# Optimization experiments

Measured on AMD Instinct MI355X. Metric: run time of the kernel, lower is better.

The kernel has to match this reference:

```python
import jax, jax.numpy as jnp
import numpy as np

B, C, I, E = 2048, 128, 16, 10            # nodes, channels, irreps_in dim (lmax=3 -> 1+3+5+7), elements
M0, K3_0, K2_0, K1_0 = 1, 23, 4, 1        # output 0e: irrep dim, num_paths per correlation order 3/2/1
M1, K3_1, K2_1, K1_1 = 3, 33, 5, 1        # output 1o


def setup_inputs() -> dict:
    key = jax.random.key(0)
    ks = jax.random.split(key, 16)
    g = lambda k, s, sc=1.0: jax.random.normal(k, s, jnp.float32) * sc
    x = g(ks[0], (B, C, I))
    # node_attrs: one-hot chemical element per node
    y = jax.nn.one_hot(jax.random.randint(ks[1], (B,), 0, E), E, dtype=jnp.float32)
    return dict(
        x=x, y=y,
        U3_0=g(ks[2], (M0, I, I, I, K3_0), 0.1), U2_0=g(ks[3], (M0, I, I, K2_0), 0.1),
        U1_0=g(ks[4], (M0, I, K1_0), 0.1),
        W3_0=g(ks[5], (E, K3_0, C), 0.05), W2_0=g(ks[6], (E, K2_0, C), 0.05),
        W1_0=g(ks[7], (E, K1_0, C), 0.05),
        U3_1=g(ks[8], (M1, I, I, I, K3_1), 0.1), U2_1=g(ks[9], (M1, I, I, K2_1), 0.1),
        U1_1=g(ks[10], (M1, I, K1_1), 0.1),
        W3_1=g(ks[11], (E, K3_1, C), 0.05), W2_1=g(ks[12], (E, K2_1, C), 0.05),
        W1_1=g(ks[13], (E, K1_1, C), 0.05),
    )


def _contraction(x, y, U3, U2, U1, W3, W2, W1):
    # MACE Contraction for one output irrep.
    # x: [b,c,i] node features, y: [b,e] one-hot element attrs.
    # main: einsum('...ik,ekc,bci,be->bc...') for correlation order 3
    wy3 = jnp.einsum("ekc,be->bkc", W3, y)                 # per-node selected weights [b,k,c]
    t = jnp.einsum("bkc,bci->bkci", wy3, x)                # [b,k,c,i]
    out = jnp.einsum("mijlk,bkci->bcmjl", U3, t)           # main contraction -> [b,c,m,j,l]
    # order 2: weighting ('...k,ekc,be->bc...') then feature contraction ('bc...i,bci->bc...')
    wy2 = jnp.einsum("ekc,be->bkc", W2, y)
    out = out + jnp.einsum("mjlk,bkc->bcmjl", U2, wy2)
    out = jnp.einsum("bcmji,bci->bcmj", out, x)            # [b,c,m,j]
    # order 1
    wy1 = jnp.einsum("ekc,be->bkc", W1, y)
    out = out + jnp.einsum("mjk,bkc->bcmj", U1, wy1)
    out = jnp.einsum("bcmi,bci->bcm", out, x)              # [b,c,m]
    return out.reshape(out.shape[0], -1)                    # [b, c*m]


def reference(x, y, U3_0, U2_0, U1_0, W3_0, W2_0, W1_0,
              U3_1, U2_1, U1_1, W3_1, W2_1, W1_1):
    out0 = _contraction(x, y, U3_0, U2_0, U1_0, W3_0, W2_0, W1_0)   # 0e -> [b, c]
    out1 = _contraction(x, y, U3_1, U2_1, U1_1, W3_1, W2_1, W1_1)   # 1o -> [b, 3c]
    return jnp.concatenate([out0, out1], axis=-1)                    # [b, 4c]
```

## Files before the change

kernel.cpp:

```cpp
#include <hip/hip_runtime.h>
#include <hip/hip_fp16.h>
#include <stdint.h>


#define BN 2048
#define CN 128
#define EN 10

#define NT3 816
#define NT2 136
#define NTT (NT3 + NT2 + 16)
#define K3_0 23
#define K3_1 33
#define K2_0 4
#define K2_1 5

#define U3S0_OFF 0
#define U3S1_OFF (K3_0*NT3)
#define U2S0_OFF (U3S1_OFF + 3*K3_1*NT3)
#define U2S1_OFF (U2S0_OFF + K2_0*NT2)
#define LISTS_OFF (U2S1_OFF + 3*K2_1*NT2)
#define CNT_OFF (LISTS_OFF + EN*BN)
#define TALL_OFF (((CNT_OFF + EN) + 3) & ~3)
#define WS_NEED_BYTES ((size_t)TALL_OFF*4 + (size_t)EN*CN*NTT*8)

#define PREP_TOT (K3_0*NT3 + 3*K3_1*NT3 + K2_0*NT2 + 3*K2_1*NT2)
#define PREP_BLOCKS ((PREP_TOT + 255) / 256)

typedef float v2f __attribute__((ext_vector_type(2)));
#define FMA2(a, b, c) __builtin_elementwise_fma((a), (b), (c))
static __device__ __forceinline__ v2f splat2(float v) { v2f r; r.x = v; r.y = v; return r; }

__global__ __launch_bounds__(256) void prep_sym(
    const float* __restrict__ U3_0, const float* __restrict__ U2_0,
    const float* __restrict__ U3_1, const float* __restrict__ U2_1,
    const float* __restrict__ yg, float* __restrict__ ws)
{
    const int bid = blockIdx.x, tid = threadIdx.x;
    if (bid < PREP_BLOCKS) {
        const int N0 = K3_0*NT3, N1 = 3*K3_1*NT3, P0 = K2_0*NT2;
        const int it = bid*256 + tid;
        if (it >= PREP_TOT) return;
        if (it < N0 + N1) {
            const float* U3; int m, k, K, t, dst;
            if (it < N0) { U3 = U3_0; K = K3_0; m = 0; k = it / NT3; t = it - k*NT3; dst = U3S0_OFF + it; }
            else { int r = it - N0; U3 = U3_1; K = K3_1; int mk = r / NT3; t = r - mk*NT3;
                   m = mk / K3_1; k = mk - m*K3_1; dst = U3S1_OFF + r; }
            int a = 0, rem = t;
            while (rem >= ((16-a)*(17-a))/2) { rem -= ((16-a)*(17-a))/2; ++a; }
            int b = a;
            while (rem >= 16-b) { rem -= 16-b; ++b; }
            const int cc = b + rem;
            #define AT3(i,j,l) U3[(size_t)(((m*16+(i))*16+(j))*16+(l))*K + k]
            float D = AT3(a,b,cc) + AT3(a,cc,b) + AT3(b,a,cc)
                    + AT3(b,cc,a) + AT3(cc,a,b) + AT3(cc,b,a);
            #undef AT3
            const int eq = (a==b) + (b==cc);
            D *= (eq==2) ? (1.f/6.f) : (eq==1) ? 0.5f : 1.f;
            ws[dst] = D;
        } else {
            const int it2 = it - (N0+N1);
            const float* U2; int m, k, K, pr, dst;
            if (it2 < P0) { U2 = U2_0; K = K2_0; m = 0; k = it2 / NT2; pr = it2 - k*NT2; dst = U2S0_OFF + it2; }
            else { int r = it2 - P0; U2 = U2_1; K = K2_1; int mk = r / NT2; pr = r - mk*NT2;
                   m = mk / K2_1; k = mk - m*K2_1; dst = U2S1_OFF + r; }
            int a = 0, rem = pr;
            while (rem >= 16-a) { rem -= 16-a; ++a; }
            const int b = a + rem;
            float D = U2[(size_t)((m*16+a)*16+b)*K + k]
                    + U2[(size_t)((m*16+b)*16+a)*K + k];
            if (a == b) D *= 0.5f;
            ws[dst] = D;
        }
    } else if (bid < PREP_BLOCKS + EN) {
        const int e = bid - PREP_BLOCKS;
        __shared__ int lcnt;
        if (tid == 0) lcnt = 0;
        __syncthreads();
        int* lists = (int*)(ws + LISTS_OFF);
        for (int b = tid; b < BN; b += 256) {
            if (yg[b*EN + e] > 0.5f) {
                int p = atomicAdd(&lcnt, 1);
                lists[e*BN + p] = b;
            }
        }
        __syncthreads();
        if (tid == 0) ((int*)(ws + CNT_OFF))[e] = lcnt;
    }
}

static __device__ __forceinline__ uint2 pack_h4(float a0, float a1, float a2, float a3) {
    __half2 lo = __floats2half2_rn(a0, a1);
    __half2 hi = __floats2half2_rn(a2, a3);
    uint2 r;
    r.x = *reinterpret_cast<const unsigned int*>(&lo);
    r.y = *reinterpret_cast<const unsigned int*>(&hi);
    return r;
}

__global__ __launch_bounds__(128) void sc_build(
    const float* __restrict__ usym, uint2* __restrict__ tall,
    const float* __restrict__ U1_0, const float* __restrict__ U1_1,
    const float* __restrict__ W3_0, const float* __restrict__ W2_0, const float* __restrict__ W1_0,
    const float* __restrict__ W3_1, const float* __restrict__ W2_1, const float* __restrict__ W1_1)
{
    const int g0 = blockIdx.x * 8;
    const int e = blockIdx.y;
    const int c = threadIdx.x;
    uint2* out8 = tall + (size_t)(e*CN + c)*NTT;

    if (g0 < NT3) {
        float w0[K3_0], w1[K3_1];
#pragma unroll
        for (int k = 0; k < K3_0; ++k) w0[k] = W3_0[(e*K3_0 + k)*CN + c];
#pragma unroll
        for (int k = 0; k < K3_1; ++k) w1[k] = W3_1[(e*K3_1 + k)*CN + c];
        const float* u0 = usym + U3S0_OFF;
        const float* u1 = usym + U3S1_OFF;
#pragma unroll 2
        for (int j = 0; j < 8; ++j) {
            const int g = g0 + j;
            float a0 = 0.f, a1 = 0.f, a2 = 0.f, a3 = 0.f;
#pragma unroll
            for (int k = 0; k < K3_0; ++k) a0 = fmaf(u0[k*NT3 + g], w0[k], a0);
#pragma unroll
            for (int k = 0; k < K3_1; ++k) {
                a1 = fmaf(u1[k*NT3 + g], w1[k], a1);
                a2 = fmaf(u1[(K3_1 + k)*NT3 + g], w1[k], a2);
                a3 = fmaf(u1[(2*K3_1 + k)*NT3 + g], w1[k], a3);
            }
            out8[g] = pack_h4(a0, a1, a2, a3);
        }
    } else if (g0 < NT3 + NT2) {
        float w0[K2_0], w1[K2_1];
#pragma unroll
        for (int k = 0; k < K2_0; ++k) w0[k] = W2_0[(e*K2_0 + k)*CN + c];
#pragma unroll
        for (int k = 0; k < K2_1; ++k) w1[k] = W2_1[(e*K2_1 + k)*CN + c];
        const float* u0 = usym + U2S0_OFF;
        const float* u1 = usym + U2S1_OFF;
#pragma unroll
        for (int j = 0; j < 8; ++j) {
            const int g = g0 + j;
            const int pr = g - NT3;
            float a0 = 0.f, a1 = 0.f, a2 = 0.f, a3 = 0.f;
#pragma unroll
            for (int k = 0; k < K2_0; ++k) a0 = fmaf(u0[k*NT2 + pr], w0[k], a0);
#pragma unroll
            for (int k = 0; k < K2_1; ++k) {
                a1 = fmaf(u1[k*NT2 + pr], w1[k], a1);
                a2 = fmaf(u1[(K2_1 + k)*NT2 + pr], w1[k], a2);
                a3 = fmaf(u1[(2*K2_1 + k)*NT2 + pr], w1[k], a3);
            }
            out8[g] = pack_h4(a0, a1, a2, a3);
        }
    } else {
        const float w10 = W1_0[e*CN + c];
        const float w11 = W1_1[e*CN + c];
#pragma unroll
        for (int j = 0; j < 8; ++j) {
            const int g = g0 + j;
            const int a = g - (NT3 + NT2);
            out8[g] = pack_h4(U1_0[a]*w10, U1_1[a]*w11,
                              U1_1[16+a]*w11, U1_1[32+a]*w11);
        }
    }
}

__global__ __launch_bounds__(128) void sc_apply(
    const float* __restrict__ xg, const float* __restrict__ ws,
    float* __restrict__ outg)
{
    const int c = blockIdx.x, e = blockIdx.y, tid = threadIdx.x;
    __shared__ uint2 Tsh[NTT];
    __shared__ v2f xs[16*128];

    const uint2* __restrict__ tG =
        (const uint2*)(ws + TALL_OFF) + (size_t)(e*CN + c)*NTT;
    for (int i = tid; i < NTT; i += 128) Tsh[i] = tG[i];

    const int* lists = (const int*)(ws + LISTS_OFF) + e*BN;
    const int cnt = ((const int*)(ws + CNT_OFF))[e];
    __syncthreads();

    for (int base = 0; base < cnt; base += 256) {
        const int s0 = base + tid, s1 = base + tid + 128;
        const bool act0 = s0 < cnt, act1 = s1 < cnt;
        const int n0 = lists[act0 ? s0 : 0];
        const int n1 = lists[act1 ? s1 : 0];
        const float4* p0 = (const float4*)(xg + ((size_t)n0*CN + c)*16);
        const float4* p1 = (const float4*)(xg + ((size_t)n1*CN + c)*16);
#pragma unroll
        for (int d = 0; d < 4; ++d) {
            const float4 v0 = p0[d]; const float4 v1 = p1[d];
            v2f w;
            w.x = v0.x; w.y = v1.x; xs[(4*d+0)*128+tid] = w;
            w.x = v0.y; w.y = v1.y; xs[(4*d+1)*128+tid] = w;
            w.x = v0.z; w.y = v1.z; xs[(4*d+2)*128+tid] = w;
            w.x = v0.w; w.y = v1.w; xs[(4*d+3)*128+tid] = w;
        }

        v2f acc0 = splat2(0.f), acc1 = acc0, acc2 = acc0, acc3 = acc0;
        int t3 = 0, t2 = NT3;
#pragma unroll 1
        for (int a = 0; a < 16; ++a) {
            const v2f xa = xs[a*128+tid];
            const uint2 t1w = Tsh[NT3 + NT2 + a];
            const float2 t1lo = __half22float2(*reinterpret_cast<const __half2*>(&t1w.x));
            const float2 t1hi = __half22float2(*reinterpret_cast<const __half2*>(&t1w.y));
            v2f tP0 = splat2(t1lo.x), tP1 = splat2(t1lo.y),
                tP2 = splat2(t1hi.x), tP3 = splat2(t1hi.y);
#pragma unroll 1
            for (int b = a; b < 16; ++b) {
                const v2f xb = xs[b*128+tid];
                const uint2 c2w = Tsh[t2]; ++t2;
                const float2 c2lo = __half22float2(*reinterpret_cast<const __half2*>(&c2w.x));
                const float2 c2hi = __half22float2(*reinterpret_cast<const __half2*>(&c2w.y));
                v2f tB0 = splat2(c2lo.x), tB1 = splat2(c2lo.y),
                    tB2 = splat2(c2hi.x), tB3 = splat2(c2hi.y);
#pragma unroll 4
                for (int cc = b; cc < 16; ++cc) {
                    const v2f xc = xs[cc*128+tid];
                    const uint2 c3w = Tsh[t3]; ++t3;
                    const float2 c3lo = __half22float2(*reinterpret_cast<const __half2*>(&c3w.x));
                    const float2 c3hi = __half22float2(*reinterpret_cast<const __half2*>(&c3w.y));
                    tB0 = FMA2(splat2(c3lo.x), xc, tB0);
                    tB1 = FMA2(splat2(c3lo.y), xc, tB1);
                    tB2 = FMA2(splat2(c3hi.x), xc, tB2);
                    tB3 = FMA2(splat2(c3hi.y), xc, tB3);
                }
                tP0 = FMA2(tB0, xb, tP0);
                tP1 = FMA2(tB1, xb, tP1);
                tP2 = FMA2(tB2, xb, tP2);
                tP3 = FMA2(tB3, xb, tP3);
            }
            acc0 = FMA2(tP0, xa, acc0);
            acc1 = FMA2(tP1, xa, acc1);
            acc2 = FMA2(tP2, xa, acc2);
            acc3 = FMA2(tP3, xa, acc3);
        }
        if (act0) {
            float* o = outg + (size_t)n0*512;
            o[c] = acc0.x;
            o[128 + c*3 + 0] = acc1.x; o[128 + c*3 + 1] = acc2.x; o[128 + c*3 + 2] = acc3.x;
        }
        if (act1) {
            float* o = outg + (size_t)n1*512;
            o[c] = acc0.y;
            o[128 + c*3 + 0] = acc1.y; o[128 + c*3 + 1] = acc2.y; o[128 + c*3 + 2] = acc3.y;
        }
    }
}

__global__ __launch_bounds__(128) void sc_main_fused(
    const float* __restrict__ xg,
    const float* __restrict__ U1_0, const float* __restrict__ U1_1,
    const float* __restrict__ W3_0, const float* __restrict__ W2_0, const float* __restrict__ W1_0,
    const float* __restrict__ W3_1, const float* __restrict__ W2_1, const float* __restrict__ W1_1,
    const float* __restrict__ ws, float* __restrict__ outg)
{
    const int c = blockIdx.x, e = blockIdx.y, tid = threadIdx.x;
    __shared__ float4 T3s[NT3];
    __shared__ float4 T2s[NT2];
    __shared__ float4 T1s[16];
    __shared__ float xs0[16*128];
    __shared__ float xs1[16*128];
    __shared__ float wk30s[K3_0], wk31s[K3_1], wk20s[K2_0], wk21s[K2_1];

    if (tid < K3_0) wk30s[tid] = W3_0[(e*K3_0 + tid)*CN + c];
    if (tid >= 32 && tid < 32 + K3_1) wk31s[tid-32] = W3_1[(e*K3_1 + (tid-32))*CN + c];
    if (tid >= 72 && tid < 72 + K2_0) wk20s[tid-72] = W2_0[(e*K2_0 + (tid-72))*CN + c];
    if (tid >= 80 && tid < 80 + K2_1) wk21s[tid-80] = W2_1[(e*K2_1 + (tid-80))*CN + c];
    __syncthreads();

    const float* u3s0 = ws + U3S0_OFF;
    const float* u3s1 = ws + U3S1_OFF;
    for (int g = tid; g < NT3/4; g += 128) {
        float4 A0 = make_float4(0,0,0,0), A1 = A0, A2 = A0, A3 = A0;
#pragma unroll
        for (int k = 0; k < K3_0; ++k) {
            const float w = wk30s[k];
            const float4 u = ((const float4*)(u3s0 + k*NT3))[g];
            A0.x = fmaf(u.x, w, A0.x); A0.y = fmaf(u.y, w, A0.y);
            A0.z = fmaf(u.z, w, A0.z); A0.w = fmaf(u.w, w, A0.w);
        }
#pragma unroll 8
        for (int k = 0; k < K3_1; ++k) {
            const float w = wk31s[k];
            const float4 ua = ((const float4*)(u3s1 + k*NT3))[g];
            A1.x = fmaf(ua.x, w, A1.x); A1.y = fmaf(ua.y, w, A1.y);
            A1.z = fmaf(ua.z, w, A1.z); A1.w = fmaf(ua.w, w, A1.w);
            const float4 ub = ((const float4*)(u3s1 + (K3_1 + k)*NT3))[g];
            A2.x = fmaf(ub.x, w, A2.x); A2.y = fmaf(ub.y, w, A2.y);
            A2.z = fmaf(ub.z, w, A2.z); A2.w = fmaf(ub.w, w, A2.w);
            const float4 uc = ((const float4*)(u3s1 + (2*K3_1 + k)*NT3))[g];
            A3.x = fmaf(uc.x, w, A3.x); A3.y = fmaf(uc.y, w, A3.y);
            A3.z = fmaf(uc.z, w, A3.z); A3.w = fmaf(uc.w, w, A3.w);
        }
        T3s[4*g+0] = make_float4(A0.x, A1.x, A2.x, A3.x);
        T3s[4*g+1] = make_float4(A0.y, A1.y, A2.y, A3.y);
        T3s[4*g+2] = make_float4(A0.z, A1.z, A2.z, A3.z);
        T3s[4*g+3] = make_float4(A0.w, A1.w, A2.w, A3.w);
    }
    const float* u2s0 = ws + U2S0_OFF;
    const float* u2s1 = ws + U2S1_OFF;
    for (int g = tid; g < NT2/4; g += 128) {
        float4 A0 = make_float4(0,0,0,0), A1 = A0, A2 = A0, A3 = A0;
#pragma unroll
        for (int k = 0; k < K2_0; ++k) {
            const float w = wk20s[k];
            const float4 u = ((const float4*)(u2s0 + k*NT2))[g];
            A0.x = fmaf(u.x, w, A0.x); A0.y = fmaf(u.y, w, A0.y);
            A0.z = fmaf(u.z, w, A0.z); A0.w = fmaf(u.w, w, A0.w);
        }
#pragma unroll
        for (int k = 0; k < K2_1; ++k) {
            const float w = wk21s[k];
            const float4 ua = ((const float4*)(u2s1 + k*NT2))[g];
            A1.x = fmaf(ua.x, w, A1.x); A1.y = fmaf(ua.y, w, A1.y);
            A1.z = fmaf(ua.z, w, A1.z); A1.w = fmaf(ua.w, w, A1.w);
            const float4 ub = ((const float4*)(u2s1 + (K2_1 + k)*NT2))[g];
            A2.x = fmaf(ub.x, w, A2.x); A2.y = fmaf(ub.y, w, A2.y);
            A2.z = fmaf(ub.z, w, A2.z); A2.w = fmaf(ub.w, w, A2.w);
            const float4 uc = ((const float4*)(u2s1 + (2*K2_1 + k)*NT2))[g];
            A3.x = fmaf(uc.x, w, A3.x); A3.y = fmaf(uc.y, w, A3.y);
            A3.z = fmaf(uc.z, w, A3.z); A3.w = fmaf(uc.w, w, A3.w);
        }
        T2s[4*g+0] = make_float4(A0.x, A1.x, A2.x, A3.x);
        T2s[4*g+1] = make_float4(A0.y, A1.y, A2.y, A3.y);
        T2s[4*g+2] = make_float4(A0.z, A1.z, A2.z, A3.z);
        T2s[4*g+3] = make_float4(A0.w, A1.w, A2.w, A3.w);
    }
    if (tid < 16) {
        const float wk10 = W1_0[e*CN + c];
        const float wk11 = W1_1[e*CN + c];
        const int j = tid;
        T1s[j] = make_float4(U1_0[j]*wk10, U1_1[j]*wk11,
                             U1_1[16+j]*wk11, U1_1[32+j]*wk11);
    }

    const int* lists = (const int*)(ws + LISTS_OFF) + e*BN;
    const int cnt = ((const int*)(ws + CNT_OFF))[e];
    __syncthreads();

    for (int base = 0; base < cnt; base += 256) {
        const int s0 = base + tid, s1 = base + tid + 128;
        const bool act0 = s0 < cnt, act1 = s1 < cnt;
        const int n0 = lists[act0 ? s0 : 0];
        const int n1 = lists[act1 ? s1 : 0];
        const float4* p0 = (const float4*)(xg + ((size_t)n0*CN + c)*16);
        const float4* p1 = (const float4*)(xg + ((size_t)n1*CN + c)*16);
#pragma unroll
        for (int d = 0; d < 4; ++d) {
            const float4 v0 = p0[d]; const float4 v1 = p1[d];
            xs0[(4*d+0)*128+tid] = v0.x; xs0[(4*d+1)*128+tid] = v0.y;
            xs0[(4*d+2)*128+tid] = v0.z; xs0[(4*d+3)*128+tid] = v0.w;
            xs1[(4*d+0)*128+tid] = v1.x; xs1[(4*d+1)*128+tid] = v1.y;
            xs1[(4*d+2)*128+tid] = v1.z; xs1[(4*d+3)*128+tid] = v1.w;
        }
        float4 acc0 = make_float4(0,0,0,0), acc1 = acc0;
        int t3 = 0, t2i = 0;
#pragma unroll 1
        for (int a = 0; a < 16; ++a) {
            const float xa0 = xs0[a*128+tid];
            const float xa1 = xs1[a*128+tid];
            float4 tP0 = T1s[a], tP1 = tP0;
#pragma unroll 1
            for (int b = a; b < 16; ++b) {
                const float xb0 = xs0[b*128+tid];
                const float xb1 = xs1[b*128+tid];
                const float4 c2v = T2s[t2i]; ++t2i;
                float4 tB0 = c2v, tB1 = c2v;
#pragma unroll 4
                for (int cc = b; cc < 16; ++cc) {
                    const float xc0 = xs0[cc*128+tid];
                    const float xc1 = xs1[cc*128+tid];
                    const float4 c3v = T3s[t3]; ++t3;
                    tB0.x = fmaf(c3v.x, xc0, tB0.x); tB0.y = fmaf(c3v.y, xc0, tB0.y);
                    tB0.z = fmaf(c3v.z, xc0, tB0.z); tB0.w = fmaf(c3v.w, xc0, tB0.w);
                    tB1.x = fmaf(c3v.x, xc1, tB1.x); tB1.y = fmaf(c3v.y, xc1, tB1.y);
                    tB1.z = fmaf(c3v.z, xc1, tB1.z); tB1.w = fmaf(c3v.w, xc1, tB1.w);
                }
                tP0.x = fmaf(tB0.x, xb0, tP0.x); tP0.y = fmaf(tB0.y, xb0, tP0.y);
                tP0.z = fmaf(tB0.z, xb0, tP0.z); tP0.w = fmaf(tB0.w, xb0, tP0.w);
                tP1.x = fmaf(tB1.x, xb1, tP1.x); tP1.y = fmaf(tB1.y, xb1, tP1.y);
                tP1.z = fmaf(tB1.z, xb1, tP1.z); tP1.w = fmaf(tB1.w, xb1, tP1.w);
            }
            acc0.x = fmaf(tP0.x, xa0, acc0.x); acc0.y = fmaf(tP0.y, xa0, acc0.y);
            acc0.z = fmaf(tP0.z, xa0, acc0.z); acc0.w = fmaf(tP0.w, xa0, acc0.w);
            acc1.x = fmaf(tP1.x, xa1, acc1.x); acc1.y = fmaf(tP1.y, xa1, acc1.y);
            acc1.z = fmaf(tP1.z, xa1, acc1.z); acc1.w = fmaf(tP1.w, xa1, acc1.w);
        }
        if (act0) {
            float* o = outg + (size_t)n0*512;
            o[c] = acc0.x;
            o[128 + c*3 + 0] = acc0.y; o[128 + c*3 + 1] = acc0.z; o[128 + c*3 + 2] = acc0.w;
        }
        if (act1) {
            float* o = outg + (size_t)n1*512;
            o[c] = acc1.x;
            o[128 + c*3 + 0] = acc1.y; o[128 + c*3 + 1] = acc1.z; o[128 + c*3 + 2] = acc1.w;
        }
    }
}

extern "C" void kernel_launch(void* const* d_in, const int* in_sizes, int n_in,
                              void* d_out, int out_size, void* d_ws, size_t ws_size,
                              hipStream_t stream) {
    const float* x = (const float*)d_in[0];
    const float* y = (const float*)d_in[1];
    const float* U3_0 = (const float*)d_in[2];
    const float* U2_0 = (const float*)d_in[3];
    const float* U1_0 = (const float*)d_in[4];
    const float* W3_0 = (const float*)d_in[5];
    const float* W2_0 = (const float*)d_in[6];
    const float* W1_0 = (const float*)d_in[7];
    const float* U3_1 = (const float*)d_in[8];
    const float* U2_1 = (const float*)d_in[9];
    const float* U1_1 = (const float*)d_in[10];
    const float* W3_1 = (const float*)d_in[11];
    const float* W2_1 = (const float*)d_in[12];
    const float* W1_1 = (const float*)d_in[13];
    float* out = (float*)d_out;
    float* ws = (float*)d_ws;

    prep_sym<<<dim3(PREP_BLOCKS + EN), 256, 0, stream>>>(U3_0, U2_0, U3_1, U2_1, y, ws);
    if (ws_size >= WS_NEED_BYTES) {
        sc_build<<<dim3(NTT/8, EN), 128, 0, stream>>>(ws, (uint2*)(ws + TALL_OFF),
                                                      U1_0, U1_1,
                                                      W3_0, W2_0, W1_0, W3_1, W2_1, W1_1);
        sc_apply<<<dim3(CN, EN), 128, 0, stream>>>(x, ws, out);
    } else {
        sc_main_fused<<<dim3(CN, EN), 128, 0, stream>>>(x, U1_0, U1_1,
                                                        W3_0, W2_0, W1_0,
                                                        W3_1, W2_1, W1_1, ws, out);
    }
}
```

Before: 209.3 us.

## Fuse symmetrization prep into build kernel and use scalar FMAs in apply

Removes the separate prep_sym launch on the main path. The build kernel now reads the raw U3/U2 tensors directly, sums the six (or two) index permutations with the per-element weights, and also builds the per-element node lists in an extra block column. The apply kernel replaces packed v2f FMAs with scalar fmaf on separate accumulators. This saves one kernel launch and the intermediate usym round trip, but the build does six times more strided U3 reads per output.

```diff
diff --git a/kernel.cpp b/kernel.cpp
--- a/kernel.cpp
+++ b/kernel.cpp
@@ -15,21 +15,236 @@
 #define K2_0 4
 #define K2_1 5
 
+#define TALL2F 20490
+#define WS2_NEED_BYTES ((size_t)TALL2F*4 + (size_t)EN*CN*NTT*8)
+
 #define U3S0_OFF 0
 #define U3S1_OFF (K3_0*NT3)
 #define U2S0_OFF (U3S1_OFF + 3*K3_1*NT3)
 #define U2S1_OFF (U2S0_OFF + K2_0*NT2)
 #define LISTS_OFF (U2S1_OFF + 3*K2_1*NT2)
 #define CNT_OFF (LISTS_OFF + EN*BN)
-#define TALL_OFF (((CNT_OFF + EN) + 3) & ~3)
-#define WS_NEED_BYTES ((size_t)TALL_OFF*4 + (size_t)EN*CN*NTT*8)
-
+#define WSF_NEED_BYTES ((size_t)(CNT_OFF + EN) * 4)
 #define PREP_TOT (K3_0*NT3 + 3*K3_1*NT3 + K2_0*NT2 + 3*K2_1*NT2)
 #define PREP_BLOCKS ((PREP_TOT + 255) / 256)
 
 typedef float v2f __attribute__((ext_vector_type(2)));
-#define FMA2(a, b, c) __builtin_elementwise_fma((a), (b), (c))
-static __device__ __forceinline__ v2f splat2(float v) { v2f r; r.x = v; r.y = v; return r; }
+
+static __device__ __forceinline__ uint2 pack_h4(float a0, float a1, float a2, float a3) {
+    __half2 lo = __floats2half2_rn(a0, a1);
+    __half2 hi = __floats2half2_rn(a2, a3);
+    uint2 r;
+    r.x = *reinterpret_cast<const unsigned int*>(&lo);
+    r.y = *reinterpret_cast<const unsigned int*>(&hi);
+    return r;
+}
+
+static __device__ __forceinline__ void acc_perm3(
+    const float* __restrict__ U3_0, const float* __restrict__ U3_1, int idx,
+    const float (&w0)[K3_0], const float (&w1)[K3_1],
+    float& s0, float& s1, float& s2, float& s3)
+{
+    const float* u0p = U3_0 + idx * K3_0;
+#pragma unroll
+    for (int k = 0; k < K3_0; ++k) s0 = fmaf(u0p[k], w0[k], s0);
+    const float* u1p = U3_1 + (size_t)idx * K3_1;
+#pragma unroll
+    for (int k = 0; k < K3_1; ++k) {
+        const float wv = w1[k];
+        s1 = fmaf(u1p[k], wv, s1);
+        s2 = fmaf(u1p[135168 + k], wv, s2);
+        s3 = fmaf(u1p[270336 + k], wv, s3);
+    }
+}
+
+__global__ __launch_bounds__(128) void build_fused(
+    const float* __restrict__ U3_0, const float* __restrict__ U2_0, const float* __restrict__ U1_0,
+    const float* __restrict__ U3_1, const float* __restrict__ U2_1, const float* __restrict__ U1_1,
+    const float* __restrict__ W3_0, const float* __restrict__ W2_0, const float* __restrict__ W1_0,
+    const float* __restrict__ W3_1, const float* __restrict__ W2_1, const float* __restrict__ W1_1,
+    const float* __restrict__ yg, float* __restrict__ ws)
+{
+    const int gx = blockIdx.x, e = blockIdx.y, tid = threadIdx.x;
+    if (gx == 121) {
+        __shared__ int lcnt;
+        if (tid == 0) lcnt = 0;
+        __syncthreads();
+        int* lists = (int*)ws;
+        for (int b = tid; b < BN; b += 128) {
+            if (yg[b * EN + e] > 0.5f) {
+                int p = atomicAdd(&lcnt, 1);
+                lists[e * BN + p] = b;
+            }
+        }
+        __syncthreads();
+        if (tid == 0) ((int*)ws)[EN * BN + e] = lcnt;
+        return;
+    }
+
+    const int g0 = gx * 8;
+    const int c = tid;
+    uint2* out8 = (uint2*)(ws + TALL2F) + (size_t)(e * CN + c) * NTT;
+
+    if (g0 < NT3) {
+        float w0[K3_0], w1[K3_1];
+#pragma unroll
+        for (int k = 0; k < K3_0; ++k) w0[k] = W3_0[(e * K3_0 + k) * CN + c];
+#pragma unroll
+        for (int k = 0; k < K3_1; ++k) w1[k] = W3_1[(e * K3_1 + k) * CN + c];
+#pragma unroll 1
+        for (int j = 0; j < 8; ++j) {
+            const int g = g0 + j;
+            int a = 0, rem = g;
+            while (rem >= ((16 - a) * (17 - a)) / 2) { rem -= ((16 - a) * (17 - a)) / 2; ++a; }
+            int b = a;
+            while (rem >= 16 - b) { rem -= 16 - b; ++b; }
+            const int cc = b + rem;
+            float s0 = 0.f, s1 = 0.f, s2 = 0.f, s3 = 0.f;
+            acc_perm3(U3_0, U3_1, (a * 16 + b) * 16 + cc, w0, w1, s0, s1, s2, s3);
+            acc_perm3(U3_0, U3_1, (a * 16 + cc) * 16 + b, w0, w1, s0, s1, s2, s3);
+            acc_perm3(U3_0, U3_1, (b * 16 + a) * 16 + cc, w0, w1, s0, s1, s2, s3);
+            acc_perm3(U3_0, U3_1, (b * 16 + cc) * 16 + a, w0, w1, s0, s1, s2, s3);
+            acc_perm3(U3_0, U3_1, (cc * 16 + a) * 16 + b, w0, w1, s0, s1, s2, s3);
+            acc_perm3(U3_0, U3_1, (cc * 16 + b) * 16 + a, w0, w1, s0, s1, s2, s3);
+            const int eq = (a == b) + (b == cc);
+            const float sc = (eq == 2) ? (1.f / 6.f) : (eq == 1) ? 0.5f : 1.f;
+            out8[g] = pack_h4(s0 * sc, s1 * sc, s2 * sc, s3 * sc);
+        }
+    } else if (g0 < NT3 + NT2) {
+        float w0[K2_0], w1[K2_1];
+#pragma unroll
+        for (int k = 0; k < K2_0; ++k) w0[k] = W2_0[(e * K2_0 + k) * CN + c];
+#pragma unroll
+        for (int k = 0; k < K2_1; ++k) w1[k] = W2_1[(e * K2_1 + k) * CN + c];
+#pragma unroll 1
+        for (int j = 0; j < 8; ++j) {
+            const int g = g0 + j;
+            int a = 0, rem = g - NT3;
+            while (rem >= 16 - a) { rem -= 16 - a; ++a; }
+            const int b = a + rem;
+            float s0 = 0.f, s1 = 0.f, s2 = 0.f, s3 = 0.f;
+#pragma unroll
+            for (int p = 0; p < 2; ++p) {
+                const int i = p ? b : a, jj = p ? a : b;
+                const float* u0p = U2_0 + (i * 16 + jj) * K2_0;
+#pragma unroll
+                for (int k = 0; k < K2_0; ++k) s0 = fmaf(u0p[k], w0[k], s0);
+                const float* u1p = U2_1 + (i * 16 + jj) * K2_1;
+#pragma unroll
+                for (int k = 0; k < K2_1; ++k) {
+                    const float wv = w1[k];
+                    s1 = fmaf(u1p[k], wv, s1);
+                    s2 = fmaf(u1p[1280 + k], wv, s2);
+                    s3 = fmaf(u1p[2560 + k], wv, s3);
+                }
+            }
+            const float sc = (a == b) ? 0.5f : 1.f;
+            out8[g] = pack_h4(s0 * sc, s1 * sc, s2 * sc, s3 * sc);
+        }
+    } else {
+        const float w10 = W1_0[e * CN + c];
+        const float w11 = W1_1[e * CN + c];
+#pragma unroll
+        for (int j = 0; j < 8; ++j) {
+            const int g = g0 + j;
+            const int a = g - (NT3 + NT2);
+            out8[g] = pack_h4(U1_0[a] * w10, U1_1[a] * w11,
+                              U1_1[16 + a] * w11, U1_1[32 + a] * w11);
+        }
+    }
+}
+
+__global__ __launch_bounds__(128) void sc_apply(
+    const float* __restrict__ xg, const float* __restrict__ ws,
+    float* __restrict__ outg)
+{
+    const int c = blockIdx.x, e = blockIdx.y, tid = threadIdx.x;
+    __shared__ uint2 Tsh[NTT];
+    __shared__ v2f xs[16 * 128];
+
+    const uint2* __restrict__ tG =
+        (const uint2*)(ws + TALL2F) + (size_t)(e * CN + c) * NTT;
+    for (int i = tid; i < NTT; i += 128) Tsh[i] = tG[i];
+
+    const int* lists = (const int*)ws + e * BN;
+    const int cnt = ((const int*)ws)[EN * BN + e];
+    __syncthreads();
+
+    for (int base = 0; base < cnt; base += 256) {
+        const int s0 = base + tid, s1 = base + tid + 128;
+        const bool act0 = s0 < cnt, act1 = s1 < cnt;
+        const int n0 = lists[act0 ? s0 : 0];
+        const int n1 = lists[act1 ? s1 : 0];
+        const float4* p0 = (const float4*)(xg + ((size_t)n0 * CN + c) * 16);
+        const float4* p1 = (const float4*)(xg + ((size_t)n1 * CN + c) * 16);
+#pragma unroll
+        for (int d = 0; d < 4; ++d) {
+            const float4 v0 = p0[d]; const float4 v1 = p1[d];
+            v2f w;
+            w.x = v0.x; w.y = v1.x; xs[(4 * d + 0) * 128 + tid] = w;
+            w.x = v0.y; w.y = v1.y; xs[(4 * d + 1) * 128 + tid] = w;
+            w.x = v0.z; w.y = v1.z; xs[(4 * d + 2) * 128 + tid] = w;
+            w.x = v0.w; w.y = v1.w; xs[(4 * d + 3) * 128 + tid] = w;
+        }
+
+        float acc00 = 0.f, acc01 = 0.f, acc10 = 0.f, acc11 = 0.f;
+        float acc20 = 0.f, acc21 = 0.f, acc30 = 0.f, acc31 = 0.f;
+        int t3 = 0, t2 = NT3;
+#pragma unroll 1
+        for (int a = 0; a < 16; ++a) {
+            const v2f xa = xs[a * 128 + tid];
+            const uint2 t1w = Tsh[NT3 + NT2 + a];
+            const __half2 t1A = *reinterpret_cast<const __half2*>(&t1w.x);
+            const __half2 t1B = *reinterpret_cast<const __half2*>(&t1w.y);
+            float tP00 = __low2float(t1A), tP10 = __high2float(t1A);
+            float tP20 = __low2float(t1B), tP30 = __high2float(t1B);
+            float tP01 = tP00, tP11 = tP10, tP21 = tP20, tP31 = tP30;
+#pragma unroll 1
+            for (int b = a; b < 16; ++b) {
+                const v2f xb = xs[b * 128 + tid];
+                const uint2 c2w = Tsh[t2]; ++t2;
+                const __half2 c2A = *reinterpret_cast<const __half2*>(&c2w.x);
+                const __half2 c2B = *reinterpret_cast<const __half2*>(&c2w.y);
+                float tB00 = __low2float(c2A), tB10 = __high2float(c2A);
+                float tB20 = __low2float(c2B), tB30 = __high2float(c2B);
+                float tB01 = tB00, tB11 = tB10, tB21 = tB20, tB31 = tB30;
+#pragma unroll 4
+                for (int cc = b; cc < 16; ++cc) {
+                    const v2f xc = xs[cc * 128 + tid];
+                    const uint2 w = Tsh[t3]; ++t3;
+                    const __half2 hA = *reinterpret_cast<const __half2*>(&w.x);
+                    const __half2 hB = *reinterpret_cast<const __half2*>(&w.y);
+                    tB00 = fmaf(__low2float(hA),  xc.x, tB00);
+                    tB01 = fmaf(__low2float(hA),  xc.y, tB01);
+                    tB10 = fmaf(__high2float(hA), xc.x, tB10);
+                    tB11 = fmaf(__high2float(hA), xc.y, tB11);
+                    tB20 = fmaf(__low2float(hB),  xc.x, tB20);
+                    tB21 = fmaf(__low2float(hB),  xc.y, tB21);
+                    tB30 = fmaf(__high2float(hB), xc.x, tB30);
+                    tB31 = fmaf(__high2float(hB), xc.y, tB31);
+                }
+                tP00 = fmaf(tB00, xb.x, tP00); tP01 = fmaf(tB01, xb.y, tP01);
+                tP10 = fmaf(tB10, xb.x, tP10); tP11 = fmaf(tB11, xb.y, tP11);
+                tP20 = fmaf(tB20, xb.x, tP20); tP21 = fmaf(tB21, xb.y, tP21);
+                tP30 = fmaf(tB30, xb.x, tP30); tP31 = fmaf(tB31, xb.y, tP31);
+            }
+            acc00 = fmaf(tP00, xa.x, acc00); acc01 = fmaf(tP01, xa.y, acc01);
+            acc10 = fmaf(tP10, xa.x, acc10); acc11 = fmaf(tP11, xa.y, acc11);
+            acc20 = fmaf(tP20, xa.x, acc20); acc21 = fmaf(tP21, xa.y, acc21);
+            acc30 = fmaf(tP30, xa.x, acc30); acc31 = fmaf(tP31, xa.y, acc31);
+        }
+        if (act0) {
+            float* o = outg + (size_t)n0 * 512;
+            o[c] = acc00;
+            o[128 + c * 3 + 0] = acc10; o[128 + c * 3 + 1] = acc20; o[128 + c * 3 + 2] = acc30;
+        }
+        if (act1) {
+            float* o = outg + (size_t)n1 * 512;
+            o[c] = acc01;
+            o[128 + c * 3 + 0] = acc11; o[128 + c * 3 + 1] = acc21; o[128 + c * 3 + 2] = acc31;
+        }
+    }
+}
 
 __global__ __launch_bounds__(256) void prep_sym(
     const float* __restrict__ U3_0, const float* __restrict__ U2_0,
@@ -89,169 +304,6 @@
     }
 }
 
-static __device__ __forceinline__ uint2 pack_h4(float a0, float a1, float a2, float a3) {
-    __half2 lo = __floats2half2_rn(a0, a1);
-    __half2 hi = __floats2half2_rn(a2, a3);
-    uint2 r;
-    r.x = *reinterpret_cast<const unsigned int*>(&lo);
-    r.y = *reinterpret_cast<const unsigned int*>(&hi);
-    return r;
-}
-
-__global__ __launch_bounds__(128) void sc_build(
-    const float* __restrict__ usym, uint2* __restrict__ tall,
-    const float* __restrict__ U1_0, const float* __restrict__ U1_1,
-    const float* __restrict__ W3_0, const float* __restrict__ W2_0, const float* __restrict__ W1_0,
-    const float* __restrict__ W3_1, const float* __restrict__ W2_1, const float* __restrict__ W1_1)
-{
-    const int g0 = blockIdx.x * 8;
-    const int e = blockIdx.y;
-    const int c = threadIdx.x;
-    uint2* out8 = tall + (size_t)(e*CN + c)*NTT;
-
-    if (g0 < NT3) {
-        float w0[K3_0], w1[K3_1];
-#pragma unroll
-        for (int k = 0; k < K3_0; ++k) w0[k] = W3_0[(e*K3_0 + k)*CN + c];
-#pragma unroll
-        for (int k = 0; k < K3_1; ++k) w1[k] = W3_1[(e*K3_1 + k)*CN + c];
-        const float* u0 = usym + U3S0_OFF;
-        const float* u1 = usym + U3S1_OFF;
-#pragma unroll 2
-        for (int j = 0; j < 8; ++j) {
-            const int g = g0 + j;
-            float a0 = 0.f, a1 = 0.f, a2 = 0.f, a3 = 0.f;
-#pragma unroll
-            for (int k = 0; k < K3_0; ++k) a0 = fmaf(u0[k*NT3 + g], w0[k], a0);
-#pragma unroll
-            for (int k = 0; k < K3_1; ++k) {
-                a1 = fmaf(u1[k*NT3 + g], w1[k], a1);
-                a2 = fmaf(u1[(K3_1 + k)*NT3 + g], w1[k], a2);
-                a3 = fmaf(u1[(2*K3_1 + k)*NT3 + g], w1[k], a3);
-            }
-            out8[g] = pack_h4(a0, a1, a2, a3);
-        }
-    } else if (g0 < NT3 + NT2) {
-        float w0[K2_0], w1[K2_1];
-#pragma unroll
-        for (int k = 0; k < K2_0; ++k) w0[k] = W2_0[(e*K2_0 + k)*CN + c];
-#pragma unroll
-        for (int k = 0; k < K2_1; ++k) w1[k] = W2_1[(e*K2_1 + k)*CN + c];
-        const float* u0 = usym + U2S0_OFF;
-        const float* u1 = usym + U2S1_OFF;
-#pragma unroll
-        for (int j = 0; j < 8; ++j) {
-            const int g = g0 + j;
-            const int pr = g - NT3;
-            float a0 = 0.f, a1 = 0.f, a2 = 0.f, a3 = 0.f;
-#pragma unroll
-            for (int k = 0; k < K2_0; ++k) a0 = fmaf(u0[k*NT2 + pr], w0[k], a0);
-#pragma unroll
-            for (int k = 0; k < K2_1; ++k) {
-                a1 = fmaf(u1[k*NT2 + pr], w1[k], a1);
-                a2 = fmaf(u1[(K2_1 + k)*NT2 + pr], w1[k], a2);
-                a3 = fmaf(u1[(2*K2_1 + k)*NT2 + pr], w1[k], a3);
-            }
-            out8[g] = pack_h4(a0, a1, a2, a3);
-        }
-    } else {
-        const float w10 = W1_0[e*CN + c];
-        const float w11 = W1_1[e*CN + c];
-#pragma unroll
-        for (int j = 0; j < 8; ++j) {
-            const int g = g0 + j;
-            const int a = g - (NT3 + NT2);
-            out8[g] = pack_h4(U1_0[a]*w10, U1_1[a]*w11,
-                              U1_1[16+a]*w11, U1_1[32+a]*w11);
-        }
-    }
-}
-
-__global__ __launch_bounds__(128) void sc_apply(
-    const float* __restrict__ xg, const float* __restrict__ ws,
-    float* __restrict__ outg)
-{
-    const int c = blockIdx.x, e = blockIdx.y, tid = threadIdx.x;
-    __shared__ uint2 Tsh[NTT];
-    __shared__ v2f xs[16*128];
-
-    const uint2* __restrict__ tG =
-        (const uint2*)(ws + TALL_OFF) + (size_t)(e*CN + c)*NTT;
-    for (int i = tid; i < NTT; i += 128) Tsh[i] = tG[i];
-
-    const int* lists = (const int*)(ws + LISTS_OFF) + e*BN;
-    const int cnt = ((const int*)(ws + CNT_OFF))[e];
-    __syncthreads();
-
-    for (int base = 0; base < cnt; base += 256) {
-        const int s0 = base + tid, s1 = base + tid + 128;
-        const bool act0 = s0 < cnt, act1 = s1 < cnt;
-        const int n0 = lists[act0 ? s0 : 0];
-        const int n1 = lists[act1 ? s1 : 0];
-        const float4* p0 = (const float4*)(xg + ((size_t)n0*CN + c)*16);
-        const float4* p1 = (const float4*)(xg + ((size_t)n1*CN + c)*16);
-#pragma unroll
-        for (int d = 0; d < 4; ++d) {
-            const float4 v0 = p0[d]; const float4 v1 = p1[d];
-            v2f w;
-            w.x = v0.x; w.y = v1.x; xs[(4*d+0)*128+tid] = w;
-            w.x = v0.y; w.y = v1.y; xs[(4*d+1)*128+tid] = w;
-            w.x = v0.z; w.y = v1.z; xs[(4*d+2)*128+tid] = w;
-            w.x = v0.w; w.y = v1.w; xs[(4*d+3)*128+tid] = w;
-        }
-
-        v2f acc0 = splat2(0.f), acc1 = acc0, acc2 = acc0, acc3 = acc0;
-        int t3 = 0, t2 = NT3;
-#pragma unroll 1
-        for (int a = 0; a < 16; ++a) {
-            const v2f xa = xs[a*128+tid];
-            const uint2 t1w = Tsh[NT3 + NT2 + a];
-            const float2 t1lo = __half22float2(*reinterpret_cast<const __half2*>(&t1w.x));
-            const float2 t1hi = __half22float2(*reinterpret_cast<const __half2*>(&t1w.y));
-            v2f tP0 = splat2(t1lo.x), tP1 = splat2(t1lo.y),
-                tP2 = splat2(t1hi.x), tP3 = splat2(t1hi.y);
-#pragma unroll 1
-            for (int b = a; b < 16; ++b) {
-                const v2f xb = xs[b*128+tid];
-                const uint2 c2w = Tsh[t2]; ++t2;
-                const float2 c2lo = __half22float2(*reinterpret_cast<const __half2*>(&c2w.x));
-                const float2 c2hi = __half22float2(*reinterpret_cast<const __half2*>(&c2w.y));
-                v2f tB0 = splat2(c2lo.x), tB1 = splat2(c2lo.y),
-                    tB2 = splat2(c2hi.x), tB3 = splat2(c2hi.y);
-#pragma unroll 4
-                for (int cc = b; cc < 16; ++cc) {
-                    const v2f xc = xs[cc*128+tid];
-                    const uint2 c3w = Tsh[t3]; ++t3;
-                    const float2 c3lo = __half22float2(*reinterpret_cast<const __half2*>(&c3w.x));
-                    const float2 c3hi = __half22float2(*reinterpret_cast<const __half2*>(&c3w.y));
-                    tB0 = FMA2(splat2(c3lo.x), xc, tB0);
-                    tB1 = FMA2(splat2(c3lo.y), xc, tB1);
-                    tB2 = FMA2(splat2(c3hi.x), xc, tB2);
-                    tB3 = FMA2(splat2(c3hi.y), xc, tB3);
-                }
-                tP0 = FMA2(tB0, xb, tP0);
-                tP1 = FMA2(tB1, xb, tP1);
-                tP2 = FMA2(tB2, xb, tP2);
-                tP3 = FMA2(tB3, xb, tP3);
-            }
-            acc0 = FMA2(tP0, xa, acc0);
-            acc1 = FMA2(tP1, xa, acc1);
-            acc2 = FMA2(tP2, xa, acc2);
-            acc3 = FMA2(tP3, xa, acc3);
-        }
-        if (act0) {
-            float* o = outg + (size_t)n0*512;
-            o[c] = acc0.x;
-            o[128 + c*3 + 0] = acc1.x; o[128 + c*3 + 1] = acc2.x; o[128 + c*3 + 2] = acc3.x;
-        }
-        if (act1) {
-            float* o = outg + (size_t)n1*512;
-            o[c] = acc0.y;
-            o[128 + c*3 + 0] = acc1.y; o[128 + c*3 + 1] = acc2.y; o[128 + c*3 + 2] = acc3.y;
-        }
-    }
-}
-
 __global__ __launch_bounds__(128) void sc_main_fused(
     const float* __restrict__ xg,
     const float* __restrict__ U1_0, const float* __restrict__ U1_1,
@@ -424,13 +476,13 @@
     float* out = (float*)d_out;
     float* ws = (float*)d_ws;
 
-    prep_sym<<<dim3(PREP_BLOCKS + EN), 256, 0, stream>>>(U3_0, U2_0, U3_1, U2_1, y, ws);
-    if (ws_size >= WS_NEED_BYTES) {
-        sc_build<<<dim3(NTT/8, EN), 128, 0, stream>>>(ws, (uint2*)(ws + TALL_OFF),
-                                                      U1_0, U1_1,
-                                                      W3_0, W2_0, W1_0, W3_1, W2_1, W1_1);
+    if (ws_size >= WS2_NEED_BYTES) {
+        build_fused<<<dim3(122, EN), 128, 0, stream>>>(
+            U3_0, U2_0, U1_0, U3_1, U2_1, U1_1,
+            W3_0, W2_0, W1_0, W3_1, W2_1, W1_1, y, ws);
         sc_apply<<<dim3(CN, EN), 128, 0, stream>>>(x, ws, out);
     } else {
+        prep_sym<<<dim3(PREP_BLOCKS + EN), 256, 0, stream>>>(U3_0, U2_0, U3_1, U2_1, y, ws);
         sc_main_fused<<<dim3(CN, EN), 128, 0, stream>>>(x, U1_0, U1_1,
                                                         W3_0, W2_0, W1_0,
                                                         W3_1, W2_1, W1_1, ws, out);
```

Result: slower. 295.8 us (+41.3%).
